# Performance work log

Measured on AMD Instinct MI355X. Metric: run time of the kernel, lower is better.

The kernel has to match this reference:

```python
import jax, jax.numpy as jnp
import numpy as np

B, N, E, H = 4, 1024, 1024, 16
D = E // H  # head dim = 64
SCALE = float(E) ** 0.5  # NOTE: original scales by embedding_dim**0.5, not head_dim


def setup_inputs() -> dict:
    key = jax.random.key(0)
    ks = jax.random.split(key, 9)
    sd = 1.0 / np.sqrt(E)
    return {
        "q": jax.random.normal(ks[0], (B, N, E), jnp.float32),
        "k": jax.random.normal(ks[1], (B, N, E), jnp.float32),
        "v": jax.random.normal(ks[2], (B, N, E), jnp.float32),
        "Wq": jax.random.normal(ks[3], (E, E), jnp.float32) * sd,
        "bq": jax.random.normal(ks[4], (E,), jnp.float32) * sd,
        "Wk": jax.random.normal(ks[5], (E, E), jnp.float32) * sd,
        "bk": jax.random.normal(ks[6], (E,), jnp.float32) * sd,
        "Wv": jax.random.normal(ks[7], (E, E), jnp.float32) * sd,
        "bv": jax.random.normal(ks[8], (E,), jnp.float32) * sd,
    }


def _split_heads(x):
    # (b, n, h*d) -> (b, h, n, d)
    b, n, _ = x.shape
    return x.reshape(b, n, H, D).transpose(0, 2, 1, 3)


def reference(q, k, v, Wq, bq, Wk, bk, Wv, bv):
    q = _split_heads(q @ Wq.T + bq)
    k = _split_heads(k @ Wk.T + bk)
    v = _split_heads(v @ Wv.T + bv)
    # full NxN scores, scaled by embedding_dim**0.5 (as in original)
    attn = jnp.einsum('bhnd,bhld->bhnl', q, k) / SCALE
    attn = jax.nn.softmax(attn, axis=-1)
    # dropout omitted (eval mode)
    # faithful to original non-standard einsum: sums attn over l, broadcasts v
    out = jnp.einsum('bhnl,bhnd->bhnd', attn, v)
    return (out, attn)
```

## Files before the change

kernel.cpp:

```cpp
#include <hip/hip_runtime.h>
#include <hip/hip_bf16.h>
#include <math.h>

#define Bc 4
#define Nc 1024
#define Ec 1024
#define Hc 16
#define Dc 64
#define Mc 4096
#define OUT0_ELEMS 4194304
#define ATTN_ELEMS 67108864ULL
#define SCRATCH_OFF 58720256
#define NTK 32

typedef __attribute__((ext_vector_type(4))) float f32x4;
typedef __attribute__((ext_vector_type(16))) float f32x16;
typedef __attribute__((ext_vector_type(8))) short s16x8;
typedef __attribute__((ext_vector_type(4))) short s16x4;

__device__ __forceinline__ short f2bf(float f) {
    union { __bf16 h; short s; } c; c.h = (__bf16)f; return c.s;
}
__device__ __forceinline__ s16x4 pk4(const f32x4 v) {
    s16x4 r;
    r[0] = f2bf(v[0]); r[1] = f2bf(v[1]); r[2] = f2bf(v[2]); r[3] = f2bf(v[3]);
    return r;
}

typedef const __attribute__((address_space(1))) char gch;
typedef __attribute__((address_space(3))) char lch;
__device__ __forceinline__ void gload16(const short* g, short* l) {
    __builtin_amdgcn_global_load_lds((gch*)g, (lch*)l, 16, 0, 0);
}

__global__ __launch_bounds__(256)
void cvt_kernel(const float* __restrict__ xq, const float* __restrict__ xk,
                const float* __restrict__ wq, const float* __restrict__ wk,
                short* __restrict__ dst)
{
    const int which = blockIdx.y;
    const float* src; size_t n, off;
    switch (which) {
      case 0:  src = xq; n = 4194304; off = 0;       break;
      case 1:  src = xk; n = 4194304; off = 4194304; break;
      case 2:  src = wq; n = 1048576; off = 8388608; break;
      default: src = wk; n = 1048576; off = 9437184; break;
    }
    const size_t i = ((size_t)blockIdx.x * 256 + threadIdx.x) * 8;
    if (i >= n) return;
    f32x4 a = *(const f32x4*)(src + i);
    f32x4 b = *(const f32x4*)(src + i + 4);
    s16x8 o;
    o[0] = f2bf(a[0]); o[1] = f2bf(a[1]); o[2] = f2bf(a[2]); o[3] = f2bf(a[3]);
    o[4] = f2bf(b[0]); o[5] = f2bf(b[1]); o[6] = f2bf(b[2]); o[7] = f2bf(b[3]);
    *(s16x8*)(dst + off + i) = o;
}

__global__ __launch_bounds__(256)
void proj_kernel(const short* __restrict__ xall, const short* __restrict__ wall,
                 const float* __restrict__ bq, const float* __restrict__ bk,
                 short* __restrict__ qws, short* __restrict__ kws)
{
    const int sel = blockIdx.z;
    const short* X = xall + (size_t)sel * 4194304;
    const short* W = wall + (size_t)sel * 1048576;
    const float* bias = (sel == 0) ? bq : bk;

    __shared__ __align__(16) short lA[3][128 * 32];
    __shared__ __align__(16) short lB[3][128 * 32];

    const int t    = threadIdx.x;
    const int lane = t & 63;
    const int w    = t >> 6;
    const int wr   = w >> 1, wc = w & 1;
    const int li   = lane & 15, g = lane >> 4;
    const int bm   = blockIdx.x * 128;
    const int bn   = blockIdx.y * 128;

    const int sr = lane >> 2;
    const int c_ = lane & 3;

    f32x4 acc[4][4];
#pragma unroll
    for (int i = 0; i < 4; ++i)
#pragma unroll
        for (int j = 0; j < 4; ++j)
            acc[i][j] = (f32x4){0.f, 0.f, 0.f, 0.f};

#define STAGE(buf, kt)                                                        \
    {                                                                         \
        const int kb = (kt) * 32;                                             \
        _Pragma("unroll")                                                     \
        for (int j = 0; j < 2; ++j) {                                         \
            const int row = w * 32 + j * 16 + sr;                             \
            const int cg  = (c_ ^ ((row >> 1) & 3)) * 8;                      \
            gload16(X + (size_t)(bm + row) * Ec + kb + cg,                    \
                    &lA[buf][(w * 32 + j * 16) * 32]);                        \
            gload16(W + (size_t)(bn + row) * Ec + kb + cg,                    \
                    &lB[buf][(w * 32 + j * 16) * 32]);                        \
        }                                                                     \
    }

    STAGE(0, 0);
    STAGE(1, 1);
    asm volatile("s_waitcnt vmcnt(4)" ::: "memory");
    __builtin_amdgcn_s_barrier();

    for (int kt = 0; kt < NTK; ++kt) {
        const int cur = kt % 3;
        if (kt + 2 < NTK) STAGE((kt + 2) % 3, kt + 2);

        s16x8 aF[4], bF[4];
#pragma unroll
        for (int mt = 0; mt < 4; ++mt) {
            const int r = wr * 64 + mt * 16 + li;
            aF[mt] = *(const s16x8*)&lA[cur][r * 32 + ((g ^ ((r >> 1) & 3)) * 8)];
        }
#pragma unroll
        for (int nt = 0; nt < 4; ++nt) {
            const int r = wc * 64 + nt * 16 + li;
            bF[nt] = *(const s16x8*)&lB[cur][r * 32 + ((g ^ ((r >> 1) & 3)) * 8)];
        }
#pragma unroll
        for (int mt = 0; mt < 4; ++mt)
#pragma unroll
            for (int nt = 0; nt < 4; ++nt)
                acc[mt][nt] = __builtin_amdgcn_mfma_f32_16x16x32_bf16(
                    aF[mt], bF[nt], acc[mt][nt], 0, 0, 0);

        if (kt + 2 < NTK) {
            asm volatile("s_waitcnt vmcnt(4)" ::: "memory");
        } else {
            asm volatile("s_waitcnt vmcnt(0)" ::: "memory");
        }
        __builtin_amdgcn_s_barrier();
    }
#undef STAGE

    short* dstBF = (sel == 0) ? qws : kws;
#pragma unroll
    for (int nt = 0; nt < 4; ++nt) {
        const int col = bn + wc * 64 + nt * 16 + li;
        const float bcol = bias[col];
        const int h = col >> 6, d = col & 63;
#pragma unroll
        for (int mt = 0; mt < 4; ++mt) {
#pragma unroll
            for (int r = 0; r < 4; ++r) {
                const int row = bm + wr * 64 + mt * 16 + g * 4 + r;
                const int bb = row >> 10, n = row & 1023;
                const size_t off = ((size_t)(bb * Hc + h) * Nc + n) * Dc + d;
                dstBF[off] = f2bf(acc[mt][nt][r] + bcol);
            }
        }
    }
}

__global__ __launch_bounds__(512, 4)
void fused_kernel(const short* __restrict__ qws, const short* __restrict__ kws,
                  float* __restrict__ attnOut,
                  const float* __restrict__ vin, const float* __restrict__ Wv,
                  const float* __restrict__ bv, float* __restrict__ out0)
{
    __shared__ __align__(16) short lA[128 * 40];
    __shared__ __align__(16) short lB[128 * 40];
    __shared__ float red[8][32];

    const int bid = blockIdx.x;
    const int t   = threadIdx.x;
    const int lane = t & 63;

    if (bid < 256) {
        const int bm = (bid & 31) * 128;
        const int bn = (bid >> 5) * 128;
        const int wid = t >> 6;
        const int wr = wid >> 2;
        const int wc = wid & 3;
        const int li = lane & 15, g = lane >> 4;

        const int srow = t >> 2;
        const int scol = (t & 3) * 8;

        const float* Xs = vin + (size_t)(bm + srow) * Ec + scol;
        const float* Ws = Wv  + (size_t)(bn + srow) * Ec + scol;

        f32x4 a0 = *(const f32x4*)(Xs);
        f32x4 a1 = *(const f32x4*)(Xs + 4);
        f32x4 b0 = *(const f32x4*)(Ws);
        f32x4 b1 = *(const f32x4*)(Ws + 4);

        f32x4 acc[4][2];
#pragma unroll
        for (int i = 0; i < 4; ++i)
#pragma unroll
            for (int j = 0; j < 2; ++j)
                acc[i][j] = (f32x4){0.f, 0.f, 0.f, 0.f};

        for (int kt = 0; kt < 32; ++kt) {
            {
                s16x8 ha, hb;
#pragma unroll
                for (int i = 0; i < 4; ++i) {
                    ha[i] = f2bf(a0[i]); ha[i + 4] = f2bf(a1[i]);
                    hb[i] = f2bf(b0[i]); hb[i + 4] = f2bf(b1[i]);
                }
                *(s16x8*)&lA[srow * 40 + scol] = ha;
                *(s16x8*)&lB[srow * 40 + scol] = hb;
            }
            __syncthreads();

            if (kt < 31) {
                const int kb = (kt + 1) * 32;
                a0 = *(const f32x4*)(Xs + kb);
                a1 = *(const f32x4*)(Xs + kb + 4);
                b0 = *(const f32x4*)(Ws + kb);
                b1 = *(const f32x4*)(Ws + kb + 4);
            }

            s16x8 aF[4], bF[2];
#pragma unroll
            for (int mt = 0; mt < 4; ++mt)
                aF[mt] = *(const s16x8*)&lA[(wr * 64 + mt * 16 + li) * 40 + g * 8];
#pragma unroll
            for (int nt = 0; nt < 2; ++nt)
                bF[nt] = *(const s16x8*)&lB[(wc * 32 + nt * 16 + li) * 40 + g * 8];
#pragma unroll
            for (int mt = 0; mt < 4; ++mt)
#pragma unroll
                for (int nt = 0; nt < 2; ++nt)
                    acc[mt][nt] = __builtin_amdgcn_mfma_f32_16x16x32_bf16(
                        aF[mt], bF[nt], acc[mt][nt], 0, 0, 0);
            __syncthreads();
        }

#pragma unroll
        for (int nt = 0; nt < 2; ++nt) {
            const int col = bn + wc * 32 + nt * 16 + li;
            const float bcol = bv[col];
            const int h = col >> 6, d = col & 63;
#pragma unroll
            for (int mt = 0; mt < 4; ++mt) {
#pragma unroll
                for (int r = 0; r < 4; ++r) {
                    const int row = bm + wr * 64 + mt * 16 + g * 4 + r;
                    const int bb = row >> 10, n = row & 1023;
                    out0[((size_t)(bb * Hc + h) * Nc + n) * Dc + d] =
                        acc[mt][nt][r] + bcol;
                }
            }
        }
        return;
    }

    const int abid = bid - 256;
    const int rb  = (abid >> 3) & 31;
    const int bh  = ((abid & 7) << 3) | (abid >> 8);
    const int w  = t >> 6;
    const int li = lane & 31;
    const int hi = lane >> 5;

    const short* Qb = qws + (size_t)bh * (Nc * Dc);
    const short* Kb = kws + (size_t)bh * (Nc * Dc);

    s16x8 qF[4];
    {
        const short* qp = Qb + (size_t)(rb * 32 + li) * Dc + hi * 8;
#pragma unroll
        for (int s = 0; s < 4; ++s)
            qF[s] = *(const s16x8*)(qp + s * 16);
    }

    f32x16 acc[4];
#pragma unroll
    for (int i = 0; i < 4; ++i) acc[i] = (f32x16)(0.f);

    const int colbase = w * 128;
#pragma unroll
    for (int ct = 0; ct < 4; ++ct) {
        const short* kp = Kb + (size_t)(colbase + ct * 32 + li) * Dc + hi * 8;
#pragma unroll
        for (int s = 0; s < 4; ++s) {
            s16x8 kf = *(const s16x8*)(kp + s * 16);
            acc[ct] = __builtin_amdgcn_mfma_f32_32x32x16_bf16(qF[s], kf, acc[ct], 0, 0, 0);
        }
    }

    const float c = 1.44269504f / 32.0f;
    float sm[16];
#pragma unroll
    for (int r = 0; r < 16; ++r) sm[r] = 0.f;
#pragma unroll
    for (int ct = 0; ct < 4; ++ct) {
#pragma unroll
        for (int r = 0; r < 16; ++r) {
            float p = __builtin_amdgcn_exp2f(acc[ct][r] * c);
            acc[ct][r] = p;
            sm[r] += p;
        }
    }
#pragma unroll
    for (int r = 0; r < 16; ++r) {
#pragma unroll
        for (int off = 1; off < 32; off <<= 1)
            sm[r] += __shfl_xor(sm[r], off);
    }

    if (li == 0) {
#pragma unroll
        for (int r = 0; r < 16; ++r)
            red[w][(r & 3) + 8 * (r >> 2) + 4 * hi] = sm[r];
    }
    __syncthreads();
#pragma unroll
    for (int r = 0; r < 16; ++r) {
        const int row = (r & 3) + 8 * (r >> 2) + 4 * hi;
        float s = red[0][row] + red[1][row] + red[2][row] + red[3][row] +
                  red[4][row] + red[5][row] + red[6][row] + red[7][row];
        sm[r] = 1.0f / s;
    }

    float* outp = attnOut + (size_t)bh * (Nc * Nc) + (size_t)(rb * 32) * Nc;
#pragma unroll
    for (int ct = 0; ct < 4; ++ct) {
        const int col = colbase + ct * 32 + li;
#pragma unroll
        for (int r = 0; r < 16; ++r) {
            const int row = (r & 3) + 8 * (r >> 2) + 4 * hi;
            __builtin_nontemporal_store(acc[ct][r] * sm[r],
                                        &outp[(size_t)row * Nc + col]);
        }
    }
}

extern "C" void kernel_launch(void* const* d_in, const int* in_sizes, int n_in,
                              void* d_out, int out_size, void* d_ws, size_t ws_size,
                              hipStream_t stream) {
    const float* q  = (const float*)d_in[0];
    const float* k  = (const float*)d_in[1];
    const float* v  = (const float*)d_in[2];
    const float* Wq = (const float*)d_in[3];
    const float* bq = (const float*)d_in[4];
    const float* Wk = (const float*)d_in[5];
    const float* bk = (const float*)d_in[6];
    const float* Wv = (const float*)d_in[7];
    const float* bv = (const float*)d_in[8];

    float* out0 = (float*)d_out;
    float* attn = (float*)d_out + OUT0_ELEMS;

    short* s16  = (short*)(attn + SCRATCH_OFF);
    short* xall = s16;
    short* wall = s16 + 8388608;

    short* qws = (short*)d_ws;
    short* kws = qws + (size_t)Mc * Ec;

    cvt_kernel<<<dim3(2048, 4), 256, 0, stream>>>(q, k, Wq, Wk, s16);
    proj_kernel<<<dim3(32, 8, 2), 256, 0, stream>>>(
        xall, wall, bq, bk, qws, kws);
    fused_kernel<<<2304, 512, 0, stream>>>(qws, kws, attn, v, Wv, bv, out0);
}
```

Baseline: 127.7 us.

## Double-buffer V projection GEMM LDS tiles with XOR swizzle and deeper prefetch

Rewrites the V-projection branch of the fused kernel to use two LDS buffers with an XOR-swizzled layout in place of padded rows, and prefetches global loads two tiles ahead. This cuts one barrier per k-step and aims to overlap LDS writes and global loads with MFMA compute, while avoiding bank conflicts without padding. It costs more registers for the extra prefetch set, which could hurt occupancy under the 512x4 launch bounds.

After: 118.8 us. 1.08x faster.

```diff
diff --git a/kernel.cpp b/kernel.cpp
--- a/kernel.cpp
+++ b/kernel.cpp
@@ -16,15 +16,9 @@
 typedef __attribute__((ext_vector_type(4))) float f32x4;
 typedef __attribute__((ext_vector_type(16))) float f32x16;
 typedef __attribute__((ext_vector_type(8))) short s16x8;
-typedef __attribute__((ext_vector_type(4))) short s16x4;
 
 __device__ __forceinline__ short f2bf(float f) {
     union { __bf16 h; short s; } c; c.h = (__bf16)f; return c.s;
-}
-__device__ __forceinline__ s16x4 pk4(const f32x4 v) {
-    s16x4 r;
-    r[0] = f2bf(v[0]); r[1] = f2bf(v[1]); r[2] = f2bf(v[2]); r[3] = f2bf(v[3]);
-    return r;
 }
 
 typedef const __attribute__((address_space(1))) char gch;
@@ -162,8 +156,8 @@
                   const float* __restrict__ vin, const float* __restrict__ Wv,
                   const float* __restrict__ bv, float* __restrict__ out0)
 {
-    __shared__ __align__(16) short lA[128 * 40];
-    __shared__ __align__(16) short lB[128 * 40];
+    __shared__ __align__(16) short lsA[2][128 * 32];
+    __shared__ __align__(16) short lsB[2][128 * 32];
     __shared__ float red[8][32];
 
     const int bid = blockIdx.x;
@@ -173,21 +167,16 @@
     if (bid < 256) {
         const int bm = (bid & 31) * 128;
         const int bn = (bid >> 5) * 128;
-        const int wid = t >> 6;
-        const int wr = wid >> 2;
-        const int wc = wid & 3;
+        const int w  = t >> 6;
+        const int wr = w >> 2;
+        const int wc = w & 3;
         const int li = lane & 15, g = lane >> 4;
 
-        const int srow = t >> 2;
-        const int scol = (t & 3) * 8;
-
-        const float* Xs = vin + (size_t)(bm + srow) * Ec + scol;
-        const float* Ws = Wv  + (size_t)(bn + srow) * Ec + scol;
-
-        f32x4 a0 = *(const f32x4*)(Xs);
-        f32x4 a1 = *(const f32x4*)(Xs + 4);
-        f32x4 b0 = *(const f32x4*)(Ws);
-        f32x4 b1 = *(const f32x4*)(Ws + 4);
+        const int r0 = t >> 2;
+        const int c2 = t & 3;
+        const float* Xs = vin + (size_t)(bm + r0) * Ec + c2 * 8;
+        const float* Ws = Wv  + (size_t)(bn + r0) * Ec + c2 * 8;
+        const int aoff = r0 * 32 + ((c2 ^ ((r0 >> 1) & 3)) * 8);
 
         f32x4 acc[4][2];
 #pragma unroll
@@ -196,42 +185,79 @@
             for (int j = 0; j < 2; ++j)
                 acc[i][j] = (f32x4){0.f, 0.f, 0.f, 0.f};
 
-        for (int kt = 0; kt < 32; ++kt) {
-            {
-                s16x8 ha, hb;
-#pragma unroll
-                for (int i = 0; i < 4; ++i) {
-                    ha[i] = f2bf(a0[i]); ha[i + 4] = f2bf(a1[i]);
-                    hb[i] = f2bf(b0[i]); hb[i + 4] = f2bf(b1[i]);
+        f32x4 eA0, eA1, eB0, eB1;
+        f32x4 oA0, oA1, oB0, oB1;
+
+#define VLOAD(a0, a1, b0, b1, kt)                                             \
+        {                                                                     \
+            const float* pa = Xs + (kt) * 32;                                 \
+            const float* pb = Ws + (kt) * 32;                                 \
+            a0 = *(const f32x4*)(pa); a1 = *(const f32x4*)(pa + 4);           \
+            b0 = *(const f32x4*)(pb); b1 = *(const f32x4*)(pb + 4);           \
+        }
+
+#define VWRITE(buf, a0, a1, b0, b1)                                           \
+        {                                                                     \
+            s16x8 ha, hb;                                                     \
+            _Pragma("unroll")                                                 \
+            for (int i = 0; i < 4; ++i) {                                     \
+                ha[i] = f2bf(a0[i]); ha[i + 4] = f2bf(a1[i]);                 \
+                hb[i] = f2bf(b0[i]); hb[i + 4] = f2bf(b1[i]);                 \
+            }                                                                 \
+            *(s16x8*)&lsA[buf][aoff] = ha;                                    \
+            *(s16x8*)&lsB[buf][aoff] = hb;                                    \
+        }
+
+#define VCOMPUTE(buf)                                                         \
+        {                                                                     \
+            s16x8 aF[4], bF[2];                                               \
+            _Pragma("unroll")                                                 \
+            for (int mt = 0; mt < 4; ++mt) {                                  \
+                const int r = wr * 64 + mt * 16 + li;                         \
+                aF[mt] = *(const s16x8*)&lsA[buf][r * 32 + ((g ^ ((r >> 1) & 3)) * 8)]; \
+            }                                                                 \
+            _Pragma("unroll")                                                 \
+            for (int nt = 0; nt < 2; ++nt) {                                  \
+                const int r = wc * 32 + nt * 16 + li;                         \
+                bF[nt] = *(const s16x8*)&lsB[buf][r * 32 + ((g ^ ((r >> 1) & 3)) * 8)]; \
+            }                                                                 \
+            _Pragma("unroll")                                                 \
+            for (int mt = 0; mt < 4; ++mt)                                    \
+                _Pragma("unroll")                                             \
+                for (int nt = 0; nt < 2; ++nt)                                \
+                    acc[mt][nt] = __builtin_amdgcn_mfma_f32_16x16x32_bf16(    \
+                        aF[mt], bF[nt], acc[mt][nt], 0, 0, 0);                \
+        }
+
+        VLOAD(eA0, eA1, eB0, eB1, 0);
+        VLOAD(oA0, oA1, oB0, oB1, 1);
+        VWRITE(0, eA0, eA1, eB0, eB1);
+        VLOAD(eA0, eA1, eB0, eB1, 2);
+        asm volatile("s_waitcnt lgkmcnt(0)" ::: "memory");
+        __builtin_amdgcn_s_barrier();
+
+        for (int tt = 0; tt < NTK; tt += 2) {
+            VCOMPUTE(0);
+            if (tt + 1 < NTK) {
+                VWRITE(1, oA0, oA1, oB0, oB1);
+                if (tt + 3 < NTK) VLOAD(oA0, oA1, oB0, oB1, tt + 3);
+            }
+            asm volatile("s_waitcnt lgkmcnt(0)" ::: "memory");
+            __builtin_amdgcn_s_barrier();
+
+            if (tt + 1 < NTK) {
+                VCOMPUTE(1);
+                if (tt + 2 < NTK) {
+                    VWRITE(0, eA0, eA1, eB0, eB1);
+                    if (tt + 4 < NTK) VLOAD(eA0, eA1, eB0, eB1, tt + 4);
                 }
-                *(s16x8*)&lA[srow * 40 + scol] = ha;
-                *(s16x8*)&lB[srow * 40 + scol] = hb;
+                asm volatile("s_waitcnt lgkmcnt(0)" ::: "memory");
+                __builtin_amdgcn_s_barrier();
             }
-            __syncthreads();
-
-            if (kt < 31) {
-                const int kb = (kt + 1) * 32;
-                a0 = *(const f32x4*)(Xs + kb);
-                a1 = *(const f32x4*)(Xs + kb + 4);
-                b0 = *(const f32x4*)(Ws + kb);
-                b1 = *(const f32x4*)(Ws + kb + 4);
-            }
-
-            s16x8 aF[4], bF[2];
-#pragma unroll
-            for (int mt = 0; mt < 4; ++mt)
-                aF[mt] = *(const s16x8*)&lA[(wr * 64 + mt * 16 + li) * 40 + g * 8];
-#pragma unroll
-            for (int nt = 0; nt < 2; ++nt)
-                bF[nt] = *(const s16x8*)&lB[(wc * 32 + nt * 16 + li) * 40 + g * 8];
-#pragma unroll
-            for (int mt = 0; mt < 4; ++mt)
-#pragma unroll
-                for (int nt = 0; nt < 2; ++nt)
-                    acc[mt][nt] = __builtin_amdgcn_mfma_f32_16x16x32_bf16(
-                        aF[mt], bF[nt], acc[mt][nt], 0, 0, 0);
-            __syncthreads();
-        }
+        }
+#undef VCOMPUTE
+#undef VWRITE
+#undef VLOAD
 
 #pragma unroll
         for (int nt = 0; nt < 2; ++nt) {
```
